# Performance work log

Measured on AMD Instinct MI355X. Metric: run time of the kernel, lower is better.

The kernel has to match this reference:

```python
import jax, jax.numpy as jnp
import numpy as np

TEMPERATURE = 0.07
EPS = 1e-12  # matches torch F.normalize default eps


def setup_inputs() -> dict:
    key = jax.random.key(0)
    k1, k2 = jax.random.split(key)
    B, D = 8192, 256
    anchor = jax.random.normal(k1, (B, D), dtype=jnp.float32)
    positive = jax.random.normal(k2, (B, D), dtype=jnp.float32)
    return {"anchor": anchor, "positive": positive}


def _l2_normalize(x):
    # torch F.normalize(p=2, dim=1): x / max(||x||, eps)
    n = jnp.sqrt(jnp.sum(x * x, axis=1, keepdims=True))
    return x / jnp.maximum(n, EPS)


def reference(anchor, positive):
    a = _l2_normalize(anchor)
    p = _l2_normalize(positive)
    # normalized vectors -> cosine similarity is just a GEMM: (B, B)
    sim = jnp.einsum('id,jd->ij', a, p)
    B = sim.shape[0]
    # hard negative mining: max over off-diagonal entries per row
    neg = jnp.where(jnp.eye(B, dtype=bool), -jnp.inf, sim)
    max_neg = jnp.max(neg, axis=-1)  # (B,)
    logits = jnp.concatenate([sim, max_neg[:, None]], axis=1) / TEMPERATURE  # (B, B+1)
    labels = jnp.arange(B)
    logp = jax.nn.log_softmax(logits, axis=-1)
    loss = -jnp.mean(jnp.take_along_axis(logp, labels[:, None], axis=1))
    return loss
```

## Files before the change

kernel.cpp:

```cpp
#include <hip/hip_runtime.h>
#include <hip/hip_bf16.h>

using floatx4 = __attribute__((ext_vector_type(4))) float;
using int4v   = __attribute__((ext_vector_type(4))) int;
using int8v   = __attribute__((ext_vector_type(8))) int;

#define TEMP_INV 14.285714285714286f
#define DD 256
#define BM 128
#define NCT 8
#define SC1 127

typedef const __attribute__((address_space(1))) unsigned int* gptr_t;
typedef __attribute__((address_space(3))) unsigned int* lptr_t;

__device__ __forceinline__ void async_cp16(const void* g, void* l) {
  __builtin_amdgcn_global_load_lds((gptr_t)g, (lptr_t)l, 16, 0, 0);
}

__global__ __launch_bounds__(256) void nrm_kernel(
    const float* __restrict__ anchor, const float* __restrict__ positive,
    unsigned char* __restrict__ a8, unsigned char* __restrict__ p8,
    float* __restrict__ diag, float* __restrict__ out) {
  if (blockIdx.x == 0 && threadIdx.x == 0) out[0] = 0.f;
  const int wave = threadIdx.x >> 6;
  const int lane = threadIdx.x & 63;
  const int row  = blockIdx.x * 4 + wave;
  const float4 va = ((const float4*)(anchor   + (size_t)row * DD))[lane];
  const float4 vp = ((const float4*)(positive + (size_t)row * DD))[lane];
  float sa = va.x * va.x + va.y * va.y + va.z * va.z + va.w * va.w;
  float sp = vp.x * vp.x + vp.y * vp.y + vp.z * vp.z + vp.w * vp.w;
#pragma unroll
  for (int m = 32; m >= 1; m >>= 1) {
    sa += __shfl_xor(sa, m, 64);
    sp += __shfl_xor(sp, m, 64);
  }
  const float ka = 1.0f / fmaxf(sqrtf(sa), 1e-12f);
  const float kp = 1.0f / fmaxf(sqrtf(sp), 1e-12f);
  int pa = __builtin_amdgcn_cvt_pk_fp8_f32(va.x * ka, va.y * ka, 0, false);
  pa     = __builtin_amdgcn_cvt_pk_fp8_f32(va.z * ka, va.w * ka, pa, true);
  int pp = __builtin_amdgcn_cvt_pk_fp8_f32(vp.x * kp, vp.y * kp, 0, false);
  pp     = __builtin_amdgcn_cvt_pk_fp8_f32(vp.z * kp, vp.w * kp, pp, true);
  ((int*)(a8 + (size_t)row * DD))[lane] = pa;
  ((int*)(p8 + (size_t)row * DD))[lane] = pp;
  float d = __builtin_amdgcn_cvt_f32_fp8(pa, 0) * __builtin_amdgcn_cvt_f32_fp8(pp, 0)
          + __builtin_amdgcn_cvt_f32_fp8(pa, 1) * __builtin_amdgcn_cvt_f32_fp8(pp, 1)
          + __builtin_amdgcn_cvt_f32_fp8(pa, 2) * __builtin_amdgcn_cvt_f32_fp8(pp, 2)
          + __builtin_amdgcn_cvt_f32_fp8(pa, 3) * __builtin_amdgcn_cvt_f32_fp8(pp, 3);
#pragma unroll
  for (int m = 32; m >= 1; m >>= 1) d += __shfl_xor(d, m, 64);
  if (lane == 0) diag[row] = d;
}

__device__ __forceinline__ int8v frag(const unsigned char* S, int row, int ks,
                                      int quad, int l16) {
  const int c0 = ks * 8 + quad * 2;
  const int4v lo = *(const int4v*)(S + row * DD + (((c0 + 0) ^ l16) << 4));
  const int4v hi = *(const int4v*)(S + row * DD + (((c0 + 1) ^ l16) << 4));
  return __builtin_shufflevector(lo, hi, 0, 1, 2, 3, 4, 5, 6, 7);
}

__global__ __launch_bounds__(512, 4) void gemm_stats(
    const unsigned char* __restrict__ a8, const unsigned char* __restrict__ p8,
    float* __restrict__ rsum, float* __restrict__ rmax, int Btot) {
  __shared__ __align__(16) unsigned char As[BM * DD];
  __shared__ __align__(16) unsigned char Bs[BM * DD];
  __shared__ float red_sum[2][BM];
  __shared__ float red_max[2][BM];

  const int t = threadIdx.x;
  const int wave = t >> 6, lane = t & 63;
  const int wm = wave & 3, wn = wave >> 2;
  const int quad = lane >> 4, l16 = lane & 15;
  const int row0    = blockIdx.y * BM;
  const int colbase = blockIdx.x * (NCT * BM);
  const bool hasdiag = ((int)(blockIdx.y >> 3) == (int)blockIdx.x);

  const int r4 = lane >> 4;
  const int cg = lane & 15;

#pragma unroll
  for (int q = 0; q < 4; ++q) {
    const int rb = q * 32 + wave * 4;
    const int r  = rb + r4;
    async_cp16(a8 + (size_t)(row0 + r) * DD + (cg ^ (r & 15)) * 16,
               &As[rb * DD]);
  }
#pragma unroll
  for (int q = 0; q < 4; ++q) {
    const int rb = q * 32 + wave * 4;
    const int r  = rb + r4;
    async_cp16(p8 + (size_t)(colbase + r) * DD + (cg ^ (r & 15)) * 16,
               &Bs[rb * DD]);
  }

  float se_run[2][4], mx_run[2][4];
#pragma unroll
  for (int a = 0; a < 2; ++a)
#pragma unroll
    for (int b = 0; b < 4; ++b) { se_run[a][b] = 0.f; mx_run[a][b] = -INFINITY; }

  for (int ct = 0; ct < NCT; ++ct) {
    __syncthreads();

    floatx4 acc[2][4];
#pragma unroll
    for (int a = 0; a < 2; ++a)
#pragma unroll
      for (int b = 0; b < 4; ++b) acc[a][b] = (floatx4){0.f, 0.f, 0.f, 0.f};

#pragma unroll
    for (int ks = 0; ks < 2; ++ks) {
      const int8v af0 = frag(As, wm * 32 + l16,      ks, quad, l16);
      const int8v af1 = frag(As, wm * 32 + 16 + l16, ks, quad, l16);
#pragma unroll
      for (int ni = 0; ni < 4; ++ni) {
        const int8v bf = frag(Bs, wn * 64 + ni * 16 + l16, ks, quad, l16);
        acc[0][ni] = __builtin_amdgcn_mfma_scale_f32_16x16x128_f8f6f4(
            af0, bf, acc[0][ni], 0, 0, 0, SC1, 0, SC1);
        acc[1][ni] = __builtin_amdgcn_mfma_scale_f32_16x16x128_f8f6f4(
            af1, bf, acc[1][ni], 0, 0, 0, SC1, 0, SC1);
      }
    }

    __syncthreads();
    if (ct + 1 < NCT) {
      const int colb = colbase + (ct + 1) * BM;
#pragma unroll
      for (int q = 0; q < 4; ++q) {
        const int rb = q * 32 + wave * 4;
        const int r  = rb + r4;
        async_cp16(p8 + (size_t)(colb + r) * DD + (cg ^ (r & 15)) * 16,
                   &Bs[rb * DD]);
      }
    }

    const int col0 = colbase + ct * BM;
    if (!hasdiag) {
#pragma unroll
      for (int mi = 0; mi < 2; ++mi)
#pragma unroll
        for (int reg = 0; reg < 4; ++reg)
#pragma unroll
          for (int ni = 0; ni < 4; ++ni) {
            const float s = acc[mi][ni][reg];
            se_run[mi][reg] += __expf(s * TEMP_INV);
            mx_run[mi][reg] = fmaxf(mx_run[mi][reg], s);
          }
    } else {
#pragma unroll
      for (int mi = 0; mi < 2; ++mi)
#pragma unroll
        for (int reg = 0; reg < 4; ++reg) {
          const int i = row0 + wm * 32 + mi * 16 + quad * 4 + reg;
#pragma unroll
          for (int ni = 0; ni < 4; ++ni) {
            const float s = acc[mi][ni][reg];
            const int j = col0 + wn * 64 + ni * 16 + l16;
            se_run[mi][reg] += __expf(s * TEMP_INV);
            mx_run[mi][reg] = fmaxf(mx_run[mi][reg], (i == j) ? -INFINITY : s);
          }
        }
    }
  }

#pragma unroll
  for (int mi = 0; mi < 2; ++mi) {
#pragma unroll
    for (int reg = 0; reg < 4; ++reg) {
      float se = se_run[mi][reg], mx = mx_run[mi][reg];
#pragma unroll
      for (int m = 1; m < 16; m <<= 1) {
        se += __shfl_xor(se, m, 64);
        mx = fmaxf(mx, __shfl_xor(mx, m, 64));
      }
      if (l16 == 0) {
        const int rb = wm * 32 + mi * 16 + quad * 4 + reg;
        red_sum[wn][rb] = se;
        red_max[wn][rb] = mx;
      }
    }
  }
  __syncthreads();
  if (t < BM) {
    rsum[(size_t)blockIdx.x * Btot + row0 + t] = red_sum[0][t] + red_sum[1][t];
    rmax[(size_t)blockIdx.x * Btot + row0 + t] = fmaxf(red_max[0][t], red_max[1][t]);
  }
}

__global__ __launch_bounds__(256) void row_loss_kernel(
    const float* __restrict__ rsum, const float* __restrict__ rmax,
    const float* __restrict__ diag, float* __restrict__ out, int Btot, int NG) {
  const int i = blockIdx.x * 256 + threadIdx.x;
  float s = 0.f, m = -INFINITY;
  for (int c = 0; c < NG; ++c) {
    s += rsum[(size_t)c * Btot + i];
    m = fmaxf(m, rmax[(size_t)c * Btot + i]);
  }
  float rl = __logf(s + __expf(m * TEMP_INV)) - diag[i] * TEMP_INV;
#pragma unroll
  for (int mm = 32; mm >= 1; mm >>= 1) rl += __shfl_xor(rl, mm, 64);
  __shared__ float red[4];
  if ((threadIdx.x & 63) == 0) red[threadIdx.x >> 6] = rl;
  __syncthreads();
  if (threadIdx.x == 0)
    atomicAdd(out, (red[0] + red[1] + red[2] + red[3]) / (float)Btot);
}

extern "C" void kernel_launch(void* const* d_in, const int* in_sizes, int n_in,
                              void* d_out, int out_size, void* d_ws, size_t ws_size,
                              hipStream_t stream) {
  const float* anchor   = (const float*)d_in[0];
  const float* positive = (const float*)d_in[1];
  const int B  = in_sizes[0] / DD;
  const int NG = B / (BM * NCT);
  const size_t BD = (size_t)B * DD;

  unsigned char* a8 = (unsigned char*)d_ws;
  unsigned char* p8 = a8 + BD;
  float* rsum  = (float*)(p8 + BD);
  float* rmax  = rsum + (size_t)NG * B;
  float* diag  = rmax + (size_t)NG * B;

  nrm_kernel<<<B / 4, 256, 0, stream>>>(anchor, positive, a8, p8, diag,
                                        (float*)d_out);
  dim3 g2(NG, B / BM);
  gemm_stats<<<g2, 512, 0, stream>>>(a8, p8, rsum, rmax, B);
  row_loss_kernel<<<B / 256, 256, 0, stream>>>(rsum, rmax, diag, (float*)d_out, B, NG);
}
```

Baseline: 97.45 us.

## Double-buffer B tiles in LDS and keep A fragments in registers

```diff
diff --git a/kernel.cpp b/kernel.cpp
--- a/kernel.cpp
+++ b/kernel.cpp
@@ -52,19 +52,24 @@
   if (lane == 0) diag[row] = d;
 }
 
-__device__ __forceinline__ int8v frag(const unsigned char* S, int row, int ks,
-                                      int quad, int l16) {
+__device__ __forceinline__ int8v fragLDS(const unsigned char* S, int row, int ks,
+                                         int quad, int l16) {
   const int c0 = ks * 8 + quad * 2;
   const int4v lo = *(const int4v*)(S + row * DD + (((c0 + 0) ^ l16) << 4));
   const int4v hi = *(const int4v*)(S + row * DD + (((c0 + 1) ^ l16) << 4));
   return __builtin_shufflevector(lo, hi, 0, 1, 2, 3, 4, 5, 6, 7);
 }
 
+__device__ __forceinline__ int8v fragG(const unsigned char* g) {
+  const int4v lo = *(const int4v*)(g);
+  const int4v hi = *(const int4v*)(g + 16);
+  return __builtin_shufflevector(lo, hi, 0, 1, 2, 3, 4, 5, 6, 7);
+}
+
 __global__ __launch_bounds__(512, 4) void gemm_stats(
     const unsigned char* __restrict__ a8, const unsigned char* __restrict__ p8,
     float* __restrict__ rsum, float* __restrict__ rmax, int Btot) {
-  __shared__ __align__(16) unsigned char As[BM * DD];
-  __shared__ __align__(16) unsigned char Bs[BM * DD];
+  __shared__ __align__(16) unsigned char Bs[2][BM * DD];
   __shared__ float red_sum[2][BM];
   __shared__ float red_max[2][BM];
 
@@ -79,19 +84,23 @@
   const int r4 = lane >> 4;
   const int cg = lane & 15;
 
-#pragma unroll
-  for (int q = 0; q < 4; ++q) {
-    const int rb = q * 32 + wave * 4;
-    const int r  = rb + r4;
-    async_cp16(a8 + (size_t)(row0 + r) * DD + (cg ^ (r & 15)) * 16,
-               &As[rb * DD]);
-  }
+  int8v a_frag[2][2];
+  {
+    const unsigned char* ab =
+        a8 + (size_t)(row0 + wm * 32 + l16) * DD + quad * 32;
+#pragma unroll
+    for (int mi = 0; mi < 2; ++mi)
+#pragma unroll
+      for (int ks = 0; ks < 2; ++ks)
+        a_frag[mi][ks] = fragG(ab + mi * 16 * DD + ks * 128);
+  }
+
 #pragma unroll
   for (int q = 0; q < 4; ++q) {
     const int rb = q * 32 + wave * 4;
     const int r  = rb + r4;
     async_cp16(p8 + (size_t)(colbase + r) * DD + (cg ^ (r & 15)) * 16,
-               &Bs[rb * DD]);
+               &Bs[0][rb * DD]);
   }
 
   float se_run[2][4], mx_run[2][4];
@@ -103,35 +112,34 @@
   for (int ct = 0; ct < NCT; ++ct) {
     __syncthreads();
 
-    floatx4 acc[2][4];
-#pragma unroll
-    for (int a = 0; a < 2; ++a)
-#pragma unroll
-      for (int b = 0; b < 4; ++b) acc[a][b] = (floatx4){0.f, 0.f, 0.f, 0.f};
-
-#pragma unroll
-    for (int ks = 0; ks < 2; ++ks) {
-      const int8v af0 = frag(As, wm * 32 + l16,      ks, quad, l16);
-      const int8v af1 = frag(As, wm * 32 + 16 + l16, ks, quad, l16);
-#pragma unroll
-      for (int ni = 0; ni < 4; ++ni) {
-        const int8v bf = frag(Bs, wn * 64 + ni * 16 + l16, ks, quad, l16);
-        acc[0][ni] = __builtin_amdgcn_mfma_scale_f32_16x16x128_f8f6f4(
-            af0, bf, acc[0][ni], 0, 0, 0, SC1, 0, SC1);
-        acc[1][ni] = __builtin_amdgcn_mfma_scale_f32_16x16x128_f8f6f4(
-            af1, bf, acc[1][ni], 0, 0, 0, SC1, 0, SC1);
-      }
-    }
-
-    __syncthreads();
     if (ct + 1 < NCT) {
       const int colb = colbase + (ct + 1) * BM;
+      unsigned char* dst = &Bs[(ct + 1) & 1][0];
 #pragma unroll
       for (int q = 0; q < 4; ++q) {
         const int rb = q * 32 + wave * 4;
         const int r  = rb + r4;
         async_cp16(p8 + (size_t)(colb + r) * DD + (cg ^ (r & 15)) * 16,
-                   &Bs[rb * DD]);
+                   dst + rb * DD);
+      }
+    }
+
+    floatx4 acc[2][4];
+#pragma unroll
+    for (int a = 0; a < 2; ++a)
+#pragma unroll
+      for (int b = 0; b < 4; ++b) acc[a][b] = (floatx4){0.f, 0.f, 0.f, 0.f};
+
+    const unsigned char* Bcur = &Bs[ct & 1][0];
+#pragma unroll
+    for (int ks = 0; ks < 2; ++ks) {
+#pragma unroll
+      for (int ni = 0; ni < 4; ++ni) {
+        const int8v bf = fragLDS(Bcur, wn * 64 + ni * 16 + l16, ks, quad, l16);
+        acc[0][ni] = __builtin_amdgcn_mfma_scale_f32_16x16x128_f8f6f4(
+            a_frag[0][ks], bf, acc[0][ni], 0, 0, 0, SC1, 0, SC1);
+        acc[1][ni] = __builtin_amdgcn_mfma_scale_f32_16x16x128_f8f6f4(
+            a_frag[1][ks], bf, acc[1][ni], 0, 0, 0, SC1, 0, SC1);
       }
     }
 
```

New measurement: 108.4 us. 11.2% more time.
